# Kernel tuning notes

Measured on AMD Instinct MI355X. Metric: run time of the kernel, lower is better.

Reference implementation:

```python
import jax, jax.numpy as jnp
import numpy as np

N = 50000   # nodes
E = 800000  # edges
D = 256     # in = hidden = out channels
R = 16      # num_relations (last index reserved for self-loops)
B = 8       # num_bases
LN_EPS = 1e-5


def setup_inputs() -> dict:
    key = jax.random.key(0)
    ks = jax.random.split(key, 20)
    s_basis = np.sqrt(2.0 / (D + D)).astype(np.float32)  # glorot-ish scale
    s_att = np.sqrt(2.0 / (R + B)).astype(np.float32)
    inp = {
        "x": jax.random.normal(ks[0], (N, D), dtype=jnp.float32),
        "edge_index": jax.random.randint(ks[1], (2, E), 0, N),
        "edge_type": jax.random.randint(ks[2], (E,), 0, R),
        "edge_attr": jax.random.uniform(ks[3], (E,), dtype=jnp.float32),
        # layer 1 params
        "basis1": jax.random.normal(ks[4], (B, D, D), dtype=jnp.float32) * s_basis,
        "att1": jax.random.normal(ks[5], (R, B), dtype=jnp.float32) * s_att,
        "root1": jax.random.normal(ks[6], (D, D), dtype=jnp.float32) * s_basis,
        "bias1": jnp.zeros((D,), dtype=jnp.float32),
        "ln1_g": jnp.ones((D,), dtype=jnp.float32),
        "ln1_b": jnp.zeros((D,), dtype=jnp.float32),
        # layer 2 params
        "basis2": jax.random.normal(ks[7], (B, D, D), dtype=jnp.float32) * s_basis,
        "att2": jax.random.normal(ks[8], (R, B), dtype=jnp.float32) * s_att,
        "root2": jax.random.normal(ks[9], (D, D), dtype=jnp.float32) * s_basis,
        "bias2": jnp.zeros((D,), dtype=jnp.float32),
        "ln2_g": jnp.ones((D,), dtype=jnp.float32),
        "ln2_b": jnp.zeros((D,), dtype=jnp.float32),
    }
    return inp


def _layer_norm(x, g, b):
    mu = jnp.mean(x, axis=-1, keepdims=True)
    var = jnp.mean(jnp.square(x - mu), axis=-1, keepdims=True)
    return (x - mu) * jax.lax.rsqrt(var + LN_EPS) * g + b


def _rgcn_layer(x, edge_index, edge_type, edge_attr, basis, att, root, bias):
    n = x.shape[0]
    r = att.shape[0]
    # W_r = sum_b a_rb V_b ; then per-relation transform of every node.
    weight = jnp.einsum('rb,bio->rio', att, basis)          # [R, D, D]
    H = jnp.einsum('ni,rio->nro', x, weight)                # [N, R, D]
    # append self-loops with relation index R-1 and confidence 1.0
    loop = jnp.arange(n, dtype=edge_index.dtype)
    src = jnp.concatenate([edge_index[0], loop])
    dst = jnp.concatenate([edge_index[1], loop])
    et = jnp.concatenate([edge_type, jnp.full((n,), r - 1, dtype=edge_type.dtype)])
    ea = jnp.concatenate([edge_attr, jnp.ones((n,), dtype=x.dtype)])
    msg = H[src, et] * ea[:, None]                          # [E+N, D]
    summ = jax.ops.segment_sum(msg, dst, num_segments=n)
    cnt = jax.ops.segment_sum(jnp.ones_like(ea), dst, num_segments=n)
    agg = summ / cnt[:, None]                               # scatter-mean (cnt >= 1 via self-loops)
    return agg + x @ root + bias


def reference(x, edge_index, edge_type, edge_attr,
              basis1, att1, root1, bias1, ln1_g, ln1_b,
              basis2, att2, root2, bias2, ln2_g, ln2_b):
    # input_proj / output_proj are Identity since in == hidden == out.
    h = x
    h_out = _rgcn_layer(h, edge_index, edge_type, edge_attr, basis1, att1, root1, bias1)
    h = jax.nn.relu(_layer_norm(h + h_out, ln1_g, ln1_b))
    h_out = _rgcn_layer(h, edge_index, edge_type, edge_attr, basis2, att2, root2, bias2)
    h = jax.nn.relu(_layer_norm(h + h_out, ln2_g, ln2_b))
    return h
```

## Files before the change

kernel.cpp:

```cpp
#include <hip/hip_runtime.h>
#include <stdint.h>

#define D 256
#define RREL 16
#define BB 8
#define K9 2304
#define LN_EPS 1e-5f

typedef __attribute__((ext_vector_type(8))) short frag8;
typedef __attribute__((ext_vector_type(4))) float floatx4;
typedef __attribute__((ext_vector_type(2))) float float2v;

__device__ __forceinline__ unsigned short f2bf(float f) {
    union { float f; uint32_t u; } v; v.f = f;
    uint32_t r = (v.u + 0x7FFFu + ((v.u >> 16) & 1u)) >> 16;
    return (unsigned short)r;
}
__device__ __forceinline__ float bf2f(unsigned short u) {
    union { uint32_t u; float f; } v; v.u = (uint32_t)u << 16;
    return v.f;
}
__device__ __forceinline__ float2v bfpair(uint32_t d) {
    union { uint32_t u; float f; } lo, hi;
    lo.u = d << 16; hi.u = d & 0xFFFF0000u;
    return (float2v){lo.f, hi.f};
}

__device__ __forceinline__ float2v pk_mul(float2v a, float2v b) {
    float2v d;
    asm("v_pk_mul_f32 %0, %1, %2" : "=v"(d) : "v"(a), "v"(b));
    return d;
}
__device__ __forceinline__ void pk_fma_lo(float2v& acc, float2v c, float2v x) {
    asm("v_pk_fma_f32 %0, %1, %2, %0 op_sel:[0,0,0] op_sel_hi:[1,0,1]"
        : "+v"(acc) : "v"(c), "v"(x));
}
__device__ __forceinline__ void pk_fma_hi(float2v& acc, float2v c, float2v x) {
    asm("v_pk_fma_f32 %0, %1, %2, %0 op_sel:[0,1,0] op_sel_hi:[1,1,1]"
        : "+v"(acc) : "v"(c), "v"(x));
}

__device__ __forceinline__ void gl2lds16(const unsigned short* g, char* l) {
    __builtin_amdgcn_global_load_lds((const __attribute__((address_space(1))) void*)g,
                                     (__attribute__((address_space(3))) void*)l, 16, 0, 0);
}

__global__ __launch_bounds__(256) void k_cvt(const float* __restrict__ src,
                                             unsigned short* __restrict__ dst, int n4) {
    int i = blockIdx.x * 256 + threadIdx.x;
    if (i >= n4) return;
    float4 v = ((const float4*)src)[i];
    ushort4 o = make_ushort4(f2bf(v.x), f2bf(v.y), f2bf(v.z), f2bf(v.w));
    ((ushort4*)dst)[i] = o;
}

__global__ void k_deg(const int* __restrict__ ei, int* __restrict__ deg, int E) {
    int e = blockIdx.x * 256 + threadIdx.x;
    if (e < E) atomicAdd(&deg[ei[E + e]], 1);
}

__global__ __launch_bounds__(256) void k_scan1(const int* __restrict__ deg,
                                               int* __restrict__ csum, int N) {
    __shared__ int sh[256];
    int n = blockIdx.x * 256 + threadIdx.x;
    sh[threadIdx.x] = (n < N) ? deg[n] : 0;
    __syncthreads();
    for (int off = 128; off > 0; off >>= 1) {
        if (threadIdx.x < off) sh[threadIdx.x] += sh[threadIdx.x + off];
        __syncthreads();
    }
    if (threadIdx.x == 0) csum[blockIdx.x] = sh[0];
}

__global__ __launch_bounds__(256) void k_scan2(int* __restrict__ csum, int nch,
                                               int* __restrict__ rowptr, int N) {
    __shared__ int sh[256];
    int tid = threadIdx.x;
    if (nch <= 256) {
        int v = (tid < nch) ? csum[tid] : 0;
        sh[tid] = v;
        __syncthreads();
        for (int off = 1; off < 256; off <<= 1) {
            int t = (tid >= off) ? sh[tid - off] : 0;
            __syncthreads();
            sh[tid] += t;
            __syncthreads();
        }
        if (tid < nch) csum[tid] = sh[tid] - v;
        if (tid == 255) rowptr[N] = sh[255];
    } else if (tid == 0) {
        int s = 0;
        for (int i = 0; i < nch; ++i) { int c = csum[i]; csum[i] = s; s += c; }
        rowptr[N] = s;
    }
}

__global__ __launch_bounds__(256) void k_scan3(const int* __restrict__ deg,
                                               const int* __restrict__ csum,
                                               int* __restrict__ rowptr,
                                               int* __restrict__ cursor,
                                               float* __restrict__ cnt, int N) {
    __shared__ int sh[256];
    int tid = threadIdx.x;
    int n = blockIdx.x * 256 + tid;
    int v = (n < N) ? deg[n] : 0;
    sh[tid] = v;
    __syncthreads();
    for (int off = 1; off < 256; off <<= 1) {
        int t = (tid >= off) ? sh[tid - off] : 0;
        __syncthreads();
        sh[tid] += t;
        __syncthreads();
    }
    int excl = sh[tid] - v + csum[blockIdx.x];
    if (n < N) {
        rowptr[n] = excl;
        cursor[n] = excl;
        cnt[n] = (float)(v + 1);
    }
}

__global__ void k_scatter(const int* __restrict__ ei, const int* __restrict__ et,
                          const float* __restrict__ ea, int* __restrict__ cursor,
                          int2* __restrict__ ep, int E) {
    int e = blockIdx.x * 256 + threadIdx.x;
    if (e >= E) return;
    int dst = ei[E + e];
    int p = atomicAdd(&cursor[dst], 1);
    ep[p] = make_int2(ei[e] | (et[e] << 24), __float_as_int(ea[e]));
}

__global__ __launch_bounds__(256) void k_prep_w(const float* __restrict__ basis,
                                                const float* __restrict__ root,
                                                unsigned short* __restrict__ Wt) {
    __shared__ float tile[64][65];
    int k0 = blockIdx.x * 64, o0 = blockIdx.y * 64;
    const float* src = (k0 < BB * D) ? (basis + (size_t)k0 * D)
                                     : (root + (size_t)(k0 - BB * D) * D);
    int tid = threadIdx.x;
#pragma unroll
    for (int t = 0; t < 16; ++t) {
        int idx = t * 256 + tid;
        int kk = idx >> 6, oo = idx & 63;
        tile[kk][oo] = src[(size_t)kk * D + o0 + oo];
    }
    __syncthreads();
#pragma unroll
    for (int t = 0; t < 16; ++t) {
        int idx = t * 256 + tid;
        int oo = idx >> 6, kk = idx & 63;
        Wt[(size_t)(o0 + oo) * K9 + k0 + kk] = f2bf(tile[kk][oo]);
    }
}

__device__ __forceinline__ void edge_fma(float2v g2[4][4], float2v c0, float2v c1,
                                         float2v c2, float2v c3,
                                         float2v x0, float2v x1) {
    pk_fma_lo(g2[0][0], c0, x0); pk_fma_lo(g2[1][0], c1, x0);
    pk_fma_lo(g2[2][0], c2, x0); pk_fma_lo(g2[3][0], c3, x0);
    pk_fma_hi(g2[0][1], c0, x0); pk_fma_hi(g2[1][1], c1, x0);
    pk_fma_hi(g2[2][1], c2, x0); pk_fma_hi(g2[3][1], c3, x0);
    pk_fma_lo(g2[0][2], c0, x1); pk_fma_lo(g2[1][2], c1, x1);
    pk_fma_lo(g2[2][2], c2, x1); pk_fma_lo(g2[3][2], c3, x1);
    pk_fma_hi(g2[0][3], c0, x1); pk_fma_hi(g2[1][3], c1, x1);
    pk_fma_hi(g2[2][3], c2, x1); pk_fma_hi(g2[3][3], c3, x1);
}

__global__ __launch_bounds__(256) void k_gather(
    const unsigned short* __restrict__ xb, const float* __restrict__ att,
    const int* __restrict__ rowptr, const int2* __restrict__ ep,
    const float* __restrict__ cnt, unsigned short* __restrict__ G,
    int n0, int rows, int N) {
    __shared__ __align__(32) float att_s[RREL * BB];
    int tid = threadIdx.x;
    if (tid < RREL * BB) att_s[tid] = att[tid];
    __syncthreads();
    int wv = tid >> 6, lane = tid & 63;
    int rloc = blockIdx.x * 4 + wv;
    if (rloc >= rows) return;
    int n = n0 + rloc;
    unsigned short* gout = G + (size_t)rloc * K9 + lane * 4;
    if (n >= N) {
        ushort4 z = make_ushort4(0, 0, 0, 0);
#pragma unroll
        for (int b = 0; b <= BB; ++b) *(ushort4*)(gout + b * D) = z;
        return;
    }
    uint2 xu = *(const uint2*)&xb[(size_t)n * D + lane * 4];
    float2v xs0 = bfpair(xu.x), xs1 = bfpair(xu.y);
    float xv[4] = {xs0.x, xs0.y, xs1.x, xs1.y};

    float2v g2[4][4];
#pragma unroll
    for (int bp = 0; bp < 4; ++bp) {
        float2v ap = {att_s[(RREL - 1) * BB + 2 * bp],
                      att_s[(RREL - 1) * BB + 2 * bp + 1]};
#pragma unroll
        for (int j = 0; j < 4; ++j) {
            float2v xs = {xv[j], xv[j]};
            g2[bp][j] = ap * xs;
        }
    }

    int e0 = rowptr[n], e1 = rowptr[n + 1];
    int e = e0;
    for (; e + 2 <= e1; e += 2) {
        int2 pa = ep[e], pb = ep[e + 1];
        uint2 udA = *(const uint2*)&xb[(size_t)(pa.x & 0xFFFFFF) * D + lane * 4];
        uint2 udB = *(const uint2*)&xb[(size_t)(pb.x & 0xFFFFFF) * D + lane * 4];
        int ra = (unsigned)pa.x >> 24, rb = (unsigned)pb.x >> 24;
        const float4* Ar = (const float4*)&att_s[ra * BB];
        const float4* Br = (const float4*)&att_s[rb * BB];
        float4 a0 = Ar[0], a1 = Ar[1];
        float4 b0 = Br[0], b1 = Br[1];
        float wa = __int_as_float(pa.y);
        float2v wa2 = {wa, wa};
        float2v ca0 = pk_mul(wa2, (float2v){a0.x, a0.y});
        float2v ca1 = pk_mul(wa2, (float2v){a0.z, a0.w});
        float2v ca2 = pk_mul(wa2, (float2v){a1.x, a1.y});
        float2v ca3 = pk_mul(wa2, (float2v){a1.z, a1.w});
        float2v xA0 = bfpair(udA.x), xA1 = bfpair(udA.y);
        edge_fma(g2, ca0, ca1, ca2, ca3, xA0, xA1);
        float wb = __int_as_float(pb.y);
        float2v wb2 = {wb, wb};
        float2v cb0 = pk_mul(wb2, (float2v){b0.x, b0.y});
        float2v cb1 = pk_mul(wb2, (float2v){b0.z, b0.w});
        float2v cb2 = pk_mul(wb2, (float2v){b1.x, b1.y});
        float2v cb3 = pk_mul(wb2, (float2v){b1.z, b1.w});
        float2v xB0 = bfpair(udB.x), xB1 = bfpair(udB.y);
        edge_fma(g2, cb0, cb1, cb2, cb3, xB0, xB1);
    }
    if (e < e1) {
        int2 pa = ep[e];
        uint2 udA = *(const uint2*)&xb[(size_t)(pa.x & 0xFFFFFF) * D + lane * 4];
        int ra = (unsigned)pa.x >> 24;
        const float4* Ar = (const float4*)&att_s[ra * BB];
        float4 a0 = Ar[0], a1 = Ar[1];
        float wa = __int_as_float(pa.y);
        float2v wa2 = {wa, wa};
        float2v ca0 = pk_mul(wa2, (float2v){a0.x, a0.y});
        float2v ca1 = pk_mul(wa2, (float2v){a0.z, a0.w});
        float2v ca2 = pk_mul(wa2, (float2v){a1.x, a1.y});
        float2v ca3 = pk_mul(wa2, (float2v){a1.z, a1.w});
        float2v xA0 = bfpair(udA.x), xA1 = bfpair(udA.y);
        edge_fma(g2, ca0, ca1, ca2, ca3, xA0, xA1);
    }
#pragma unroll
    for (int bp = 0; bp < 4; ++bp) {
        ushort4 o0 = make_ushort4(f2bf(g2[bp][0].x), f2bf(g2[bp][1].x),
                                  f2bf(g2[bp][2].x), f2bf(g2[bp][3].x));
        *(ushort4*)(gout + (2 * bp) * D) = o0;
        ushort4 o1 = make_ushort4(f2bf(g2[bp][0].y), f2bf(g2[bp][1].y),
                                  f2bf(g2[bp][2].y), f2bf(g2[bp][3].y));
        *(ushort4*)(gout + (2 * bp + 1) * D) = o1;
    }
    float cn = cnt[n];
    ushort4 o = make_ushort4(f2bf(cn * xv[0]), f2bf(cn * xv[1]),
                             f2bf(cn * xv[2]), f2bf(cn * xv[3]));
    *(ushort4*)(gout + BB * D) = o;
}

__global__ __launch_bounds__(256, 4) void k_gemm(
    const unsigned short* __restrict__ G, const unsigned short* __restrict__ Wt,
    const float* __restrict__ hin, const float* __restrict__ cnt,
    const float* __restrict__ bias, const float* __restrict__ gln,
    const float* __restrict__ bln, float* __restrict__ hout,
    unsigned short* __restrict__ houtb, int n0, int N) {
    __shared__ __align__(16) char smem[40960];
    char* Asb = smem;
    char* Bsb = smem + 8192;
    float* ps   = (float*)smem;
    float* pq   = ps + 256;
    float* mu_s = ps + 512;
    float* rs_s = ps + 576;

    int tid = threadIdx.x;
    int wv = tid >> 6, lane = tid & 63;
    int quad = lane >> 4, l16 = lane & 15;
    int grow = blockIdx.x * 64;
    int nb = n0 + grow;

    const unsigned short* gA[2]; char* lA[2];
#pragma unroll
    for (int t = 0; t < 2; ++t) {
        int c = (wv * 2 + t) * 64 + lane;
        int arow = c >> 3, aslot = c & 7;
        gA[t] = G + (size_t)(grow + arow) * K9 + ((aslot ^ (arow & 7)) << 3);
        lA[t] = Asb + ((wv * 2 + t) << 10);
    }
    const unsigned short* gB[8]; char* lB[8];
#pragma unroll
    for (int t = 0; t < 8; ++t) {
        int c = (wv * 8 + t) * 64 + lane;
        int brow = c >> 3, bslot = c & 7;
        gB[t] = Wt + (size_t)brow * K9 + ((bslot ^ (brow & 7)) << 3);
        lB[t] = Bsb + ((wv * 8 + t) << 10);
    }

    floatx4 acc[4][4];
#pragma unroll
    for (int mf = 0; mf < 4; ++mf)
#pragma unroll
        for (int nf = 0; nf < 4; ++nf) acc[mf][nf] = (floatx4){0.f, 0.f, 0.f, 0.f};

    for (int it = 0; it < K9 / 64; ++it) {
        __syncthreads();
        int koff = it * 64;
#pragma unroll
        for (int t = 0; t < 2; ++t) gl2lds16(gA[t] + koff, lA[t]);
#pragma unroll
        for (int t = 0; t < 8; ++t) gl2lds16(gB[t] + koff, lB[t]);
        __syncthreads();
#pragma unroll
        for (int kc = 0; kc < 2; ++kc) {
            int g = kc * 4 + quad;
            frag8 a[4], b[4];
#pragma unroll
            for (int mf = 0; mf < 4; ++mf) {
                int arow = mf * 16 + l16;
                a[mf] = *(const frag8*)(Asb + arow * 128 + ((g ^ (arow & 7)) << 4));
            }
#pragma unroll
            for (int nf = 0; nf < 4; ++nf) {
                int brow = wv * 64 + nf * 16 + l16;
                b[nf] = *(const frag8*)(Bsb + brow * 128 + ((g ^ (brow & 7)) << 4));
            }
#pragma unroll
            for (int mf = 0; mf < 4; ++mf)
#pragma unroll
                for (int nf = 0; nf < 4; ++nf)
                    acc[mf][nf] = __builtin_amdgcn_mfma_f32_16x16x32_bf16(
                        a[mf], b[nf], acc[mf][nf], 0, 0, 0);
        }
    }
    __syncthreads();

    int col[4]; float bic[4];
#pragma unroll
    for (int nf = 0; nf < 4; ++nf) {
        col[nf] = wv * 64 + nf * 16 + l16;
        bic[nf] = bias[col[nf]];
    }
#pragma unroll
    for (int mf = 0; mf < 4; ++mf) {
#pragma unroll
        for (int r = 0; r < 4; ++r) {
            int row = mf * 16 + quad * 4 + r;
            int n = nb + row;
            float s = 0.f, sq = 0.f;
            if (n < N) {
                float inv = 1.0f / cnt[n];
                const float* hp = hin + (size_t)n * D;
#pragma unroll
                for (int nf = 0; nf < 4; ++nf) {
                    float v = acc[mf][nf][r] * inv + hp[col[nf]] + bic[nf];
                    acc[mf][nf][r] = v;
                    s += v; sq += v * v;
                }
            }
            s += __shfl_xor(s, 1); sq += __shfl_xor(sq, 1);
            s += __shfl_xor(s, 2); sq += __shfl_xor(sq, 2);
            s += __shfl_xor(s, 4); sq += __shfl_xor(sq, 4);
            s += __shfl_xor(s, 8); sq += __shfl_xor(sq, 8);
            if (l16 == 0) {
                ps[row * 4 + wv] = s;
                pq[row * 4 + wv] = sq;
            }
        }
    }
    __syncthreads();
    if (tid < 64) {
        float s  = ps[tid * 4] + ps[tid * 4 + 1] + ps[tid * 4 + 2] + ps[tid * 4 + 3];
        float sq = pq[tid * 4] + pq[tid * 4 + 1] + pq[tid * 4 + 2] + pq[tid * 4 + 3];
        float mu = s * (1.f / D);
        mu_s[tid] = mu;
        rs_s[tid] = rsqrtf(sq * (1.f / D) - mu * mu + LN_EPS);
    }
    __syncthreads();

    float gc[4], bc[4];
#pragma unroll
    for (int nf = 0; nf < 4; ++nf) {
        gc[nf] = gln[col[nf]];
        bc[nf] = bln[col[nf]];
    }
#pragma unroll
    for (int mf = 0; mf < 4; ++mf) {
#pragma unroll
        for (int r = 0; r < 4; ++r) {
            int row = mf * 16 + quad * 4 + r;
            int n = nb + row;
            if (n >= N) continue;
            float mu = mu_s[row], rs = rs_s[row];
            float* op = hout + (size_t)n * D;
#pragma unroll
            for (int nf = 0; nf < 4; ++nf) {
                float o = fmaxf((acc[mf][nf][r] - mu) * rs * gc[nf] + bc[nf], 0.f);
                op[col[nf]] = o;
                if (houtb) houtb[(size_t)n * D + col[nf]] = f2bf(o);
            }
        }
    }
}

extern "C" void kernel_launch(void* const* d_in, const int* in_sizes, int n_in,
                              void* d_out, int out_size, void* d_ws, size_t ws_size,
                              hipStream_t stream) {
    const float* x      = (const float*)d_in[0];
    const int*   ei     = (const int*)d_in[1];
    const int*   et     = (const int*)d_in[2];
    const float* ea     = (const float*)d_in[3];
    const float* basis1 = (const float*)d_in[4];
    const float* att1   = (const float*)d_in[5];
    const float* root1  = (const float*)d_in[6];
    const float* bias1  = (const float*)d_in[7];
    const float* g1     = (const float*)d_in[8];
    const float* b1     = (const float*)d_in[9];
    const float* basis2 = (const float*)d_in[10];
    const float* att2   = (const float*)d_in[11];
    const float* root2  = (const float*)d_in[12];
    const float* bias2  = (const float*)d_in[13];
    const float* g2     = (const float*)d_in[14];
    const float* b2     = (const float*)d_in[15];
    float* out = (float*)d_out;

    int N = in_sizes[0] / D;
    int E = in_sizes[2];
    int nch = (N + 255) / 256;
    int Mp = ((N + 63) / 64) * 64;
    int T = Mp / 64;

    char* p = (char*)d_ws;
    size_t used = 0;
    auto alloc = [&](size_t bytes) {
        char* q = p;
        size_t a = (bytes + 255) & ~(size_t)255;
        p += a; used += a;
        return q;
    };
    float*          h1     = (float*)alloc((size_t)N * D * 4);
    unsigned short* xb     = (unsigned short*)alloc((size_t)N * D * 2);
    unsigned short* h1b    = (unsigned short*)alloc((size_t)N * D * 2);
    unsigned short* Wt     = (unsigned short*)alloc((size_t)K9 * D * 2);
    int*            deg    = (int*)alloc((size_t)N * 4);
    int*            rowptr = (int*)alloc((size_t)(N + 1) * 4);
    int*            cursor = (int*)alloc((size_t)N * 4);
    float*          cnt    = (float*)alloc((size_t)N * 4);
    int2*           ep     = (int2*)alloc((size_t)E * 8);
    int*            csum   = (int*)alloc((size_t)nch * 4);
    size_t remain = (ws_size > used + 256) ? (ws_size - used - 256) : 0;
    size_t tile_bytes = (size_t)64 * K9 * 2;
    int ct = (int)(remain / tile_bytes);
    if (ct < 1) ct = 1;
    if (ct > T) ct = T;
    unsigned short* G = (unsigned short*)alloc((size_t)ct * tile_bytes);

    hipMemsetAsync(deg, 0, (size_t)N * 4, stream);
    int gE = (E + 255) / 256;
    k_deg<<<gE, 256, 0, stream>>>(ei, deg, E);
    k_scan1<<<nch, 256, 0, stream>>>(deg, csum, N);
    k_scan2<<<1, 256, 0, stream>>>(csum, nch, rowptr, N);
    k_scan3<<<nch, 256, 0, stream>>>(deg, csum, rowptr, cursor, cnt, N);
    k_scatter<<<gE, 256, 0, stream>>>(ei, et, ea, cursor, ep, E);
    k_cvt<<<(N * D / 4 + 255) / 256, 256, 0, stream>>>(x, xb, N * D / 4);

    const float* bas[2]  = {basis1, basis2};
    const float* attp[2] = {att1, att2};
    const float* rt[2]   = {root1, root2};
    const float* bi[2]   = {bias1, bias2};
    const float* lg[2]   = {g1, g2};
    const float* lb[2]   = {b1, b2};
    const unsigned short* gin[2] = {xb, h1b};
    const float* hres[2] = {x, h1};
    float*          hof[2] = {h1, out};
    unsigned short* hob[2] = {h1b, nullptr};

    for (int L = 0; L < 2; ++L) {
        k_prep_w<<<dim3(K9 / 64, D / 64), 256, 0, stream>>>(bas[L], rt[L], Wt);
        for (int c0 = 0; c0 < T; c0 += ct) {
            int tiles = (T - c0 < ct) ? (T - c0) : ct;
            int rows = tiles * 64;
            int n0 = c0 * 64;
            k_gather<<<rows / 4, 256, 0, stream>>>(gin[L], attp[L], rowptr, ep,
                                                   cnt, G, n0, rows, N);
            k_gemm<<<tiles, 256, 0, stream>>>(G, Wt, hres[L], cnt, bi[L], lg[L], lb[L],
                                              hof[L], hob[L], n0, N);
        }
    }
}
```

Baseline: 724.8 us.

## Double-buffer LDS tiles in the GEMM main loop to overlap loads with MFMA

Restructures the k_gemm K-loop into a two-stage ping-pong pipeline. The next K-tile's global-to-LDS copy is issued before computing on the current buffer, which removes one barrier per iteration and hides load latency behind MFMA work. LDS use doubles to 80KB, and launch bounds drop from 4 to 2 blocks per CU, so occupancy-based latency hiding is reduced in exchange.

```diff
diff --git a/kernel.cpp b/kernel.cpp
--- a/kernel.cpp
+++ b/kernel.cpp
@@ -6,6 +6,8 @@
 #define BB 8
 #define K9 2304
 #define LN_EPS 1e-5f
+#define NT (K9 / 64)
+#define BUFB 40960
 
 typedef __attribute__((ext_vector_type(8))) short frag8;
 typedef __attribute__((ext_vector_type(4))) float floatx4;
@@ -260,15 +262,13 @@
     *(ushort4*)(gout + BB * D) = o;
 }
 
-__global__ __launch_bounds__(256, 4) void k_gemm(
+__global__ __launch_bounds__(256, 2) void k_gemm(
     const unsigned short* __restrict__ G, const unsigned short* __restrict__ Wt,
     const float* __restrict__ hin, const float* __restrict__ cnt,
     const float* __restrict__ bias, const float* __restrict__ gln,
     const float* __restrict__ bln, float* __restrict__ hout,
     unsigned short* __restrict__ houtb, int n0, int N) {
-    __shared__ __align__(16) char smem[40960];
-    char* Asb = smem;
-    char* Bsb = smem + 8192;
+    __shared__ __align__(16) char smem[2 * BUFB];
     float* ps   = (float*)smem;
     float* pq   = ps + 256;
     float* mu_s = ps + 512;
@@ -286,7 +286,7 @@
         int c = (wv * 2 + t) * 64 + lane;
         int arow = c >> 3, aslot = c & 7;
         gA[t] = G + (size_t)(grow + arow) * K9 + ((aslot ^ (arow & 7)) << 3);
-        lA[t] = Asb + ((wv * 2 + t) << 10);
+        lA[t] = smem + ((wv * 2 + t) << 10);
     }
     const unsigned short* gB[8]; char* lB[8];
 #pragma unroll
@@ -294,7 +294,7 @@
         int c = (wv * 8 + t) * 64 + lane;
         int brow = c >> 3, bslot = c & 7;
         gB[t] = Wt + (size_t)brow * K9 + ((bslot ^ (brow & 7)) << 3);
-        lB[t] = Bsb + ((wv * 8 + t) << 10);
+        lB[t] = smem + 8192 + ((wv * 8 + t) << 10);
     }
 
     floatx4 acc[4][4];
@@ -303,14 +303,16 @@
 #pragma unroll
         for (int nf = 0; nf < 4; ++nf) acc[mf][nf] = (floatx4){0.f, 0.f, 0.f, 0.f};
 
-    for (int it = 0; it < K9 / 64; ++it) {
-        __syncthreads();
+    auto STAGE = [&](int it, int soff) {
         int koff = it * 64;
 #pragma unroll
-        for (int t = 0; t < 2; ++t) gl2lds16(gA[t] + koff, lA[t]);
-#pragma unroll
-        for (int t = 0; t < 8; ++t) gl2lds16(gB[t] + koff, lB[t]);
-        __syncthreads();
+        for (int t = 0; t < 2; ++t) gl2lds16(gA[t] + koff, lA[t] + soff);
+#pragma unroll
+        for (int t = 0; t < 8; ++t) gl2lds16(gB[t] + koff, lB[t] + soff);
+    };
+    auto COMPUTE = [&](int soff) {
+        const char* Ab = smem + soff;
+        const char* Bb = Ab + 8192;
 #pragma unroll
         for (int kc = 0; kc < 2; ++kc) {
             int g = kc * 4 + quad;
@@ -318,12 +320,12 @@
 #pragma unroll
             for (int mf = 0; mf < 4; ++mf) {
                 int arow = mf * 16 + l16;
-                a[mf] = *(const frag8*)(Asb + arow * 128 + ((g ^ (arow & 7)) << 4));
+                a[mf] = *(const frag8*)(Ab + arow * 128 + ((g ^ (arow & 7)) << 4));
             }
 #pragma unroll
             for (int nf = 0; nf < 4; ++nf) {
                 int brow = wv * 64 + nf * 16 + l16;
-                b[nf] = *(const frag8*)(Bsb + brow * 128 + ((g ^ (brow & 7)) << 4));
+                b[nf] = *(const frag8*)(Bb + brow * 128 + ((g ^ (brow & 7)) << 4));
             }
 #pragma unroll
             for (int mf = 0; mf < 4; ++mf)
@@ -332,8 +334,18 @@
                     acc[mf][nf] = __builtin_amdgcn_mfma_f32_16x16x32_bf16(
                         a[mf], b[nf], acc[mf][nf], 0, 0, 0);
         }
-    }
-    __syncthreads();
+    };
+
+    STAGE(0, 0);
+    __syncthreads();
+    for (int it = 0; it < NT; it += 2) {
+        STAGE(it + 1, BUFB);
+        COMPUTE(0);
+        __syncthreads();
+        if (it + 2 < NT) STAGE(it + 2, 0);
+        COMPUTE(BUFB);
+        __syncthreads();
+    }
 
     int col[4]; float bic[4];
 #pragma unroll
```

Result: slower. 740.7 us (+2.2%).
